# Kernel optimization log

Hardware: AMD Instinct MI355X
Metric: run time of the kernel (lower is better)

Reference implementation:

```python
import jax, jax.numpy as jnp
import numpy as np

RC = 5.0
P = 6
N_ATOM = 4
N_AXIS = 8
EPS = 1e-5
C_RES = 0.89442719  # sqrt(0.8)
C_NEW = 0.4472      # ~sqrt(0.2)
BESSEL_PREF = float(np.sqrt(2.0 / RC))


def poly_cutoff(x):
    # nequip-style PolynomialCutoff, p=6
    xr = x / RC
    p = float(P)
    out = (1.0
           - (p + 1.0) * (p + 2.0) / 2.0 * xr ** P
           + p * (p + 2.0) * xr ** (P + 1)
           - p * (p + 1.0) / 2.0 * xr ** (P + 2))
    return jnp.where(xr < 1.0, out, 0.0)


def bessel(x, w):
    # x: [E], w: [n_basis] (trainable n*pi weights)
    return BESSEL_PREF * jnp.sin(w * x[:, None] / RC) / x[:, None]


def layer_norm(x, g, b):
    m = jnp.mean(x, axis=-1, keepdims=True)
    v = jnp.var(x, axis=-1, keepdims=True)
    return (x - m) * jax.lax.rsqrt(v + EPS) * g + b


def mlp3(x, W1, b1, W2, b2, W3, b3):
    # FFN: hidden block (linear-tanh-linear) + tanh + final linear
    h = jnp.tanh(x @ W1 + b1)
    h = jnp.tanh(h @ W2 + b2)
    return h @ W3 + b3


def resnet3(x, W1, b1, W2, b2, W3, b3):
    # ResNet: residual added where in/out dims match (final 64->64 linear)
    h = jnp.tanh(x @ W1 + b1)
    h = h @ W2 + b2
    return jnp.tanh(h) @ W3 + b3 + h


def seg_mean(x, idx, n):
    s = jax.ops.segment_sum(x, idx, num_segments=n)
    c = jax.ops.segment_sum(jnp.ones((x.shape[0],), x.dtype), idx, num_segments=n)
    c = jnp.maximum(c, 1.0).reshape((n,) + (1,) * (x.ndim - 1))
    return s / c


def setup_inputs() -> dict:
    key = jax.random.key(0)
    ks = iter(jax.random.split(key, 64))
    N, E, E2 = 40000, 320000, 160000
    NB, NR, NS, NA = 16, 64, 16, 8
    D = NA * NS  # 128 = n_hidden
    L = 2
    f32 = jnp.float32

    def nrm(shape, s=0.05):
        return jax.random.normal(next(ks), shape, dtype=f32) * s

    inp = {}
    inp['atom_types'] = jax.random.randint(next(ks), (N,), 0, N_ATOM, dtype=jnp.int32)
    ev = jax.random.normal(next(ks), (E, 3), dtype=f32)
    inp['env_vectors'] = ev
    inp['env_length'] = jnp.linalg.norm(ev, axis=-1) + 0.1
    inp['edge_length'] = jax.random.uniform(next(ks), (E2,), dtype=f32) * 4.0 + 0.5
    inp['env_index'] = jax.random.randint(next(ks), (2, E), 0, N, dtype=jnp.int32)
    inp['edge_index'] = jax.random.randint(next(ks), (2, E2), 0, N, dtype=jnp.int32)
    inp['bessel_w'] = jnp.arange(1, NB + 1, dtype=f32) * jnp.pi
    A = 2 * N_ATOM + NB  # 24
    inp['sr_W1'], inp['sr_b1'] = nrm((A, 64)), nrm((64,))
    inp['sr_W2'], inp['sr_b2'] = nrm((64, 64)), nrm((64,))
    inp['sr_W3'], inp['sr_b3'] = nrm((64, NS)), nrm((NS,))
    inp['rd_W1'], inp['rd_b1'] = nrm((A, 64)), nrm((64,))
    inp['rd_W2'], inp['rd_b2'] = nrm((64, 64)), nrm((64,))
    inp['rd_W3'], inp['rd_b3'] = nrm((64, NR)), nrm((NR,))
    inp['ne_emb_W'], inp['ne_emb_b'] = nrm((NR, D)), nrm((D,))
    inp['ne_nln_g'], inp['ne_nln_b'] = jnp.ones((D,), f32), jnp.zeros((D,), f32)
    inp['ne_eln_g'], inp['ne_eln_b'] = jnp.ones((NR,), f32), jnp.zeros((NR,), f32)
    inp['ly_emb_W'], inp['ly_emb_b'] = nrm((L, NR, D)), nrm((L, D))
    inp['ly_hid_W1'], inp['ly_hid_b1'] = nrm((L, 2 * D, 128)), nrm((L, 128))
    inp['ly_hid_W2'], inp['ly_hid_b2'] = nrm((L, 128, 128)), nrm((L, 128))
    inp['ly_hid_W3'], inp['ly_hid_b3'] = nrm((L, 128, D)), nrm((L, D))
    inp['ly_rdl_W1'], inp['ly_rdl_b1'] = nrm((L, NR + D, 64)), nrm((L, 64))
    inp['ly_rdl_W2'], inp['ly_rdl_b2'] = nrm((L, 64, 64)), nrm((L, 64))
    inp['ly_rdl_W3'], inp['ly_rdl_b3'] = nrm((L, 64, NR)), nrm((L, NR))
    inp['ly_nln_g'], inp['ly_nln_b'] = jnp.ones((L, D), f32), jnp.zeros((L, D), f32)
    inp['ly_eln_g'], inp['ly_eln_b'] = jnp.ones((L, NR), f32), jnp.zeros((L, NR), f32)
    return inp


def reference(atom_types, env_vectors, env_length, edge_length, env_index, edge_index,
              bessel_w,
              sr_W1, sr_b1, sr_W2, sr_b2, sr_W3, sr_b3,
              rd_W1, rd_b1, rd_W2, rd_b2, rd_W3, rd_b3,
              ne_emb_W, ne_emb_b, ne_nln_g, ne_nln_b, ne_eln_g, ne_eln_b,
              ly_emb_W, ly_emb_b,
              ly_hid_W1, ly_hid_b1, ly_hid_W2, ly_hid_b2, ly_hid_W3, ly_hid_b3,
              ly_rdl_W1, ly_rdl_b1, ly_rdl_W2, ly_rdl_b2, ly_rdl_W3, ly_rdl_b3,
              ly_nln_g, ly_nln_b, ly_eln_g, ly_eln_b):
    N = atom_types.shape[0]
    oh = jax.nn.one_hot(atom_types, N_ATOM, dtype=env_vectors.dtype)
    # atom_attr[index].transpose(1,0).reshape(E,-1) == concat of the two endpoints' one-hots
    env_attr = jnp.concatenate([oh[env_index[0]], oh[env_index[1]]], -1)   # [E, 2*n_atom]
    edge_attr = jnp.concatenate([oh[edge_index[0]], oh[edge_index[1]]], -1)
    ud_env = poly_cutoff(env_length)[:, None]    # [E, 1]
    ud_edge = poly_cutoff(edge_length)[:, None]  # [E2, 1]
    feat_env = jnp.concatenate([env_attr, ud_env * bessel(env_length, bessel_w)], -1)
    feat_edge = jnp.concatenate([edge_attr, ud_edge * bessel(edge_length, bessel_w)], -1)
    env_sqrt = mlp3(feat_env, sr_W1, sr_b1, sr_W2, sr_b2, sr_W3, sr_b3) * ud_env  # [E, n_sqrt]
    env_radial = layer_norm(mlp3(feat_env, rd_W1, rd_b1, rd_W2, rd_b2, rd_W3, rd_b3), ne_eln_g, ne_eln_b) * ud_env
    edge_radial = layer_norm(mlp3(feat_edge, rd_W1, rd_b1, rd_W2, rd_b2, rd_W3, rd_b3), ne_eln_g, ne_eln_b) * ud_edge
    # SE(2) aggregation: msg = [env_sqrt | ud * env_vectors]; outer product per node
    msg = env_sqrt[:, :, None] * (ud_env * env_vectors)[:, None, :]  # [E, n_sqrt, 3]
    agg = seg_mean(msg, env_index[1], N)                             # [N, n_sqrt, 3]
    gram = jnp.einsum('nds,nes->nde', agg, agg)[:, :, :N_AXIS]       # [N, n_sqrt, n_axis]
    node_emb = layer_norm(gram.reshape(N, -1), ne_nln_g, ne_nln_b)   # [N, D]
    env_hidden = (env_radial @ ne_emb_W + ne_emb_b) * (node_emb[env_index[1]] + node_emb[env_index[0]]) * 0.5
    edge_hidden = (edge_radial @ ne_emb_W + ne_emb_b) * (node_emb[edge_index[1]] + node_emb[edge_index[0]]) * 0.5
    for l in range(ly_emb_W.shape[0]):
        env_weight = env_radial @ ly_emb_W[l] + ly_emb_b[l]  # [E, D]
        agg2 = seg_mean(env_weight * node_emb[env_index[1]], env_index[1], N)
        node_emb = C_RES * node_emb + C_NEW * layer_norm(agg2, ly_nln_g[l], ly_nln_b[l])
        env_hidden = mlp3(jnp.concatenate([node_emb[env_index[0]], env_hidden], -1),
                          ly_hid_W1[l], ly_hid_b1[l], ly_hid_W2[l], ly_hid_b2[l], ly_hid_W3[l], ly_hid_b3[l])
        edge_hidden = mlp3(jnp.concatenate([node_emb[edge_index[0]], edge_hidden], -1),
                           ly_hid_W1[l], ly_hid_b1[l], ly_hid_W2[l], ly_hid_b2[l], ly_hid_W3[l], ly_hid_b3[l])
        env_radial = C_RES * env_radial + C_NEW * ud_env * layer_norm(
            resnet3(jnp.concatenate([env_radial, env_hidden], -1),
                    ly_rdl_W1[l], ly_rdl_b1[l], ly_rdl_W2[l], ly_rdl_b2[l], ly_rdl_W3[l], ly_rdl_b3[l]),
            ly_eln_g[l], ly_eln_b[l])
        edge_radial = C_RES * edge_radial + C_NEW * ud_edge * layer_norm(
            resnet3(jnp.concatenate([edge_radial, edge_hidden], -1),
                    ly_rdl_W1[l], ly_rdl_b1[l], ly_rdl_W2[l], ly_rdl_b2[l], ly_rdl_W3[l], ly_rdl_b3[l]),
            ly_eln_g[l], ly_eln_b[l])
    return env_radial, edge_radial, node_emb, env_hidden, edge_hidden
```

## Files before the change

kernel.cpp:

```cpp
#include <hip/hip_runtime.h>
#include <math.h>

#define C_RES 0.89442719f
#define C_NEW 0.4472f
#define LN_EPS 1e-5f
#define BESSEL_PREF 0.6324555320336759f
#define RC_INV 0.2f

typedef __attribute__((ext_vector_type(8))) short short8;
typedef __attribute__((ext_vector_type(8))) unsigned short u16x8;
typedef __attribute__((ext_vector_type(16))) float f32x16;

__device__ __forceinline__ float fast_tanh(float x) {
  float t = fminf(3.0f, fmaxf(-3.0f, x));
  float t2 = t * t;
  float num = t * fmaf(t2, 10.0f, 105.0f);
  float den = fmaf(t2, fmaf(t2, 1.0f, 45.0f), 105.0f);
  return num * __builtin_amdgcn_rcpf(den);
}

__device__ __forceinline__ unsigned short f2b(float f) {
  __bf16 h = (__bf16)f;
  return __builtin_bit_cast(unsigned short, h);
}
// ... 330 lines not shown
      float s = v0 + v1, ss = v0*v0 + v1*v1;
      #pragma unroll
      for (int o = 1; o <= 16; o <<= 1) {
        s  += __shfl_xor(s, o);
        ss += __shfl_xor(ss, o);
      }
      const float m   = s * (1.0f/64.0f);
      const float inv = rsqrtf(ss * (1.0f/64.0f) - m*m + LN_EPS);
      const int row32 = (q & 3) + 8*(q >> 2) + 4*(lane >> 5);
      const int rloc  = wave*32 + row32;
      const int row   = base + rloc;
      if (row < nrows) {
        const float u = udl[rloc];
        radial_out[(size_t)row*64 + cl]      = ((v0 - m)*inv*eg0 + eb0) * u;
        radial_out[(size_t)row*64 + 32 + cl] = ((v1 - m)*inv*eg1 + eb1) * u;
      }
    }
  }

  if (has_sr) {
    {
      const float bv0 = srb1[cl], bv1 = srb1[32 + cl];
      #pragma unroll
      for (int q = 0; q < 16; ++q) { acc0[q] = bv0; acc1[q] = bv1; }
    }
    #pragma unroll
    for (int kc = 0; kc < 2; ++kc) {
      const short8 a  = *(const short8*)&afrag[(kc*3 + wave)*512 + swz(lane, kc)*8];
      const short8 w0 = *(const short8*)&wlds[(20 + kc*2 + 0)*512 + lane*8];
      const short8 w1 = *(const short8*)&wlds[(20 + kc*2 + 1)*512 + lane*8];
      acc0 = __builtin_amdgcn_mfma_f32_32x32x16_bf16(a, w0, acc0, 0, 0, 0);
      acc1 = __builtin_amdgcn_mfma_f32_32x32x16_bf16(a, w1, acc1, 0, 0, 0);
    }
    FEAT_TRANS(6, acc0, acc1);

    {
      const float bv0 = srb2[cl], bv1 = srb2[32 + cl];
      #pragma unroll
      for (int q = 0; q < 16; ++q) { acc0[q] = bv0; acc1[q] = bv1; }
    }
    #pragma unroll
    for (int kc = 0; kc < 4; ++kc) {
      const short8 a  = *(const short8*)&afrag[((6 + kc*3) + wave)*512 + swz(lane, kc)*8];
      const short8 w0 = *(const short8*)&wlds[(24 + kc*2 + 0)*512 + lane*8];
      const short8 w1 = *(const short8*)&wlds[(24 + kc*2 + 1)*512 + lane*8];
      acc0 = __builtin_amdgcn_mfma_f32_32x32x16_bf16(a, w0, acc0, 0, 0, 0);
      acc1 = __builtin_amdgcn_mfma_f32_32x32x16_bf16(a, w1, acc1, 0, 0, 0);
    }
    FEAT_TRANS(18, acc0, acc1);

    {
      const float bv0 = (cl < 16) ? srb3[cl] : 0.0f;
      #pragma unroll
      for (int q = 0; q < 16; ++q) acc0[q] = bv0;
    }
    #pragma unroll
    for (int kc = 0; kc < 4; ++kc) {
      const short8 a  = *(const short8*)&afrag[((18 + kc*3) + wave)*512 + swz(lane, kc)*8];
      const short8 w0 = *(const short8*)&wlds[(32 + kc)*512 + lane*8];
      acc0 = __builtin_amdgcn_mfma_f32_32x32x16_bf16(a, w0, acc0, 0, 0, 0);
    }
    if (cl < 16) {
      #pragma unroll
      for (int q = 0; q < 16; ++q) {
        const int row32 = (q & 3) + 8*(q >> 2) + 4*(lane >> 5);
        const int rloc  = wave*32 + row32;
        const int row   = base + rloc;
        if (row < nrows) msgbuf[(size_t)row*20 + cl] = acc0[q] * udl[rloc];
      }
    }
  }
}


__launch_bounds__(256)
__global__ void msg_gather_kernel(int N, const int* __restrict__ eoff,
                                  const int* __restrict__ perm,
                                  const float* __restrict__ msgbuf,
                                  float* __restrict__ aggS)
{
  const int w = (blockIdx.x * 256 + threadIdx.x) >> 6;
  const int lane = threadIdx.x & 63;
  if (w >= N) return;
  const int s = eoff[w], e = eoff[w + 1];
  const int d = lane / 3, c = lane - d * 3;
  float acc = 0.0f;
  for (int j = s; j < e; ++j) {
    const int ed = perm[j];
    if (lane < 48)
      acc += msgbuf[(size_t)ed*20 + d] * msgbuf[(size_t)ed*20 + 16 + c];
  }
  if (lane < 48) aggS[(size_t)w*48 + lane] = acc;
}


__device__ __forceinline__ void block128_stats(float x, float& m, float& inv, float* red) {
  float s = x, ss = x*x;
  #pragma unroll
  for (int o = 32; o; o >>= 1) { s += __shfl_down(s, o); ss += __shfl_down(ss, o); }
  const int t = threadIdx.x;
  if ((t & 63) == 0) { red[(t >> 6)*2] = s; red[(t >> 6)*2 + 1] = ss; }
  __syncthreads();
  const float S = red[0] + red[2], SS = red[1] + red[3];
  m = S * (1.0f/128.0f);
  const float var = SS * (1.0f/128.0f) - m*m;
  inv = rsqrtf(var + LN_EPS);
}

__launch_bounds__(128)
__global__ void node_emb_kernel(int N, const float* __restrict__ aggS,
                                const int* __restrict__ ecnt,
                                const float* __restrict__ g, const float* __restrict__ b,
                                float* __restrict__ node_emb)
{
  const int n = blockIdx.x, t = threadIdx.x;
  __shared__ float S[48];
  __shared__ float red[4];
  if (t < 48) S[t] = aggS[(size_t)n*48 + t];
  __syncthreads();
  const float ic = 1.0f / fmaxf((float)ecnt[n], 1.0f);
  const int d = t >> 3, e = t & 7;
  const float x = (S[d*3+0]*S[e*3+0] + S[d*3+1]*S[e*3+1] + S[d*3+2]*S[e*3+2]) * ic * ic;
  float m, inv;
  block128_stats(x, m, inv, red);
  node_emb[(size_t)n*128 + t] = (x - m)*inv*g[t] + b[t];
}


__launch_bounds__(256)
__global__ void agg_gather_kernel(int N, const int* __restrict__ eoff,
                                  const int* __restrict__ perm,
                                  const float* __restrict__ radial,
                                  float* __restrict__ mean_r)
{
  const int w = (blockIdx.x * 256 + threadIdx.x) >> 6;
  const int lane = threadIdx.x & 63;
  if (w >= N) return;
  const int s = eoff[w], e = eoff[w + 1];
  float acc = 0.0f;
  for (int j = s; j < e; ++j) {
    const int ed = perm[j];
    acc += radial[(size_t)ed * 64 + lane];
  }
  const float inv = 1.0f / fmaxf((float)(e - s), 1.0f);
  mean_r[(size_t)w * 64 + lane] = acc * inv;
}


__launch_bounds__(256)
__global__ void node_update_gemm(
    int N, const float* __restrict__ mean_r, const int* __restrict__ ecnt,
    const float* __restrict__ W, const float* __restrict__ bias,
    const float* __restrict__ g, const float* __restrict__ b,
    float* __restrict__ node_emb)
{
  __shared__ __align__(16) float lw[64*128];
  __shared__ float lm[32][65];
  const int tid = threadIdx.x;
  const int base = blockIdx.x * 32;

  for (int i = tid; i < 8192; i += 256) lw[i] = W[i];
  {
    const int rr0 = tid >> 6, k = tid & 63;
    for (int rr = rr0; rr < 32; rr += 4) {
      const int n = base + rr;
      lm[rr][k] = (n < N) ? mean_r[(size_t)n*64 + k] : 0.0f;
    }
  }
  __syncthreads();

  const int r0 = (tid >> 5) * 4, j0 = (tid & 31) * 4;
  float acc[4][4];
  #pragma unroll
  for (int j = 0; j < 4; ++j) {
    const float bj = bias[j0 + j];
    acc[0][j] = bj; acc[1][j] = bj; acc[2][j] = bj; acc[3][j] = bj;
  }
  for (int k = 0; k < 64; ++k) {
    const float4 w = *(const float4*)&lw[k*128 + j0];
    const float s0 = lm[r0][k],   s1 = lm[r0+1][k];
    const float s2 = lm[r0+2][k], s3 = lm[r0+3][k];
    acc[0][0] += s0*w.x; acc[0][1] += s0*w.y; acc[0][2] += s0*w.z; acc[0][3] += s0*w.w;
    acc[1][0] += s1*w.x; acc[1][1] += s1*w.y; acc[1][2] += s1*w.z; acc[1][3] += s1*w.w;
    acc[2][0] += s2*w.x; acc[2][1] += s2*w.y; acc[2][2] += s2*w.z; acc[2][3] += s2*w.w;
    acc[3][0] += s3*w.x; acc[3][1] += s3*w.y; acc[3][2] += s3*w.z; acc[3][3] += s3*w.w;
  }

  const float g0 = g[j0], g1 = g[j0+1], g2 = g[j0+2], g3 = g[j0+3];
  const float bb0 = b[j0], bb1 = b[j0+1], bb2 = b[j0+2], bb3 = b[j0+3];
  #pragma unroll
  for (int i = 0; i < 4; ++i) {
    const int n = base + r0 + i;
    if (n >= N) continue;
    const float mask = (ecnt[n] > 0) ? 1.0f : 0.0f;
    const float4 old = *(const float4*)&node_emb[(size_t)n*128 + j0];
    const float x0 = old.x * acc[i][0] * mask;
    const float x1 = old.y * acc[i][1] * mask;
    const float x2 = old.z * acc[i][2] * mask;
    const float x3 = old.w * acc[i][3] * mask;
    float s = x0 + x1 + x2 + x3;
    float ss = x0*x0 + x1*x1 + x2*x2 + x3*x3;
    #pragma unroll
    for (int o = 1; o <= 16; o <<= 1) {
      s  += __shfl_xor(s, o);
      ss += __shfl_xor(ss, o);
    }
    const float m = s * (1.0f/128.0f);
    const float inv = rsqrtf(ss * (1.0f/128.0f) - m*m + LN_EPS);
    float4 o4;
    o4.x = C_RES*old.x + C_NEW*((x0 - m)*inv*g0 + bb0);
    o4.y = C_RES*old.y + C_NEW*((x1 - m)*inv*g1 + bb1);
    o4.z = C_RES*old.z + C_NEW*((x2 - m)*inv*g2 + bb2);
    o4.w = C_RES*old.w + C_NEW*((x3 - m)*inv*g3 + bb3);
    *(float4*)&node_emb[(size_t)n*128 + j0] = o4;
  }
}


__launch_bounds__(192)
__global__ void emb_mfma(
    int g1, int n1, const float* __restrict__ radial1, const int* __restrict__ idx1,
    float* __restrict__ out1,
    int n2, const float* __restrict__ radial2, const int* __restrict__ idx2,
    float* __restrict__ out2,
    const unsigned short* __restrict__ wpck, const float* __restrict__ bias,
    const float* __restrict__ node_emb)
{
  __shared__ __align__(16) unsigned short afrag[12*512];
  __shared__ __align__(16) unsigned short wlds[16*512];
  __shared__ int i0l[96], i1l[96];

  const int tid = threadIdx.x, lane = tid & 63, wave = tid >> 6;
  const int cl = lane & 31;

  int blk = blockIdx.x;
  int nrows; const float* radial; const int* idx; float* out;
  if (blk < g1) { nrows = n1; radial = radial1; idx = idx1; out = out1; }
  else { blk -= g1; nrows = n2; radial = radial2; idx = idx2; out = out2; }
  const int base = blk * 96;

  for (int i = tid; i < 1024; i += 192)
    *(u16x8*)&wlds[i*8] = *(const u16x8*)&wpck[i*8];

  {
    const int r = tid >> 1, h = tid & 1;
    int rowg = base + r;
    if (rowg >= nrows) rowg = nrows - 1;
    if (h == 0) { i0l[r] = idx[rowg]; i1l[r] = idx[nrows + rowg]; }
    const float* rsrc = radial + (size_t)rowg * 64;
    #pragma unroll
    for (int g = 0; g < 4; ++g) {
      const int k = h*32 + g*8;
      const u16x8 w = cvt8(rsrc + k);
      const int kc = k >> 4;
      const int s_ = (r & 31) + 32*((k >> 3) & 1);
      *(u16x8*)&afrag[(kc*3 + (r>>5))*512 + swz(s_, kc)*8] = w;
    }
  }
  __syncthreads();

  f32x16 acc0, acc1, acc2, acc3;
  {
    const float bv0 = bias[cl], bv1 = bias[32+cl];
    const float bv2 = bias[64+cl], bv3 = bias[96+cl];
    #pragma unroll
    for (int q = 0; q < 16; ++q) { acc0[q]=bv0; acc1[q]=bv1; acc2[q]=bv2; acc3[q]=bv3; }
  }
  #pragma unroll
  for (int kc = 0; kc < 4; ++kc) {
    const short8 a  = *(const short8*)&afrag[(kc*3 + wave)*512 + swz(lane, kc)*8];
    const short8 w0 = *(const short8*)&wlds[(kc*4 + 0)*512 + lane*8];
    const short8 w1 = *(const short8*)&wlds[(kc*4 + 1)*512 + lane*8];
    const short8 w2 = *(const short8*)&wlds[(kc*4 + 2)*512 + lane*8];
    const short8 w3 = *(const short8*)&wlds[(kc*4 + 3)*512 + lane*8];
    acc0 = __builtin_amdgcn_mfma_f32_32x32x16_bf16(a, w0, acc0, 0, 0, 0);
    acc1 = __builtin_amdgcn_mfma_f32_32x32x16_bf16(a, w1, acc1, 0, 0, 0);
    acc2 = __builtin_amdgcn_mfma_f32_32x32x16_bf16(a, w2, acc2, 0, 0, 0);
    acc3 = __builtin_amdgcn_mfma_f32_32x32x16_bf16(a, w3, acc3, 0, 0, 0);
  }

  #pragma unroll
  for (int q = 0; q < 16; ++q) {
    const int row32 = (q & 3) + 8*(q >> 2) + 4*(lane >> 5);
    const int rloc  = wave*32 + row32;
    const int row   = base + rloc;
    if (row >= nrows) continue;
    const float* n0 = node_emb + (size_t)i0l[rloc]*128;
    const float* n1 = node_emb + (size_t)i1l[rloc]*128;
    float* op = out + (size_t)row*128;
    op[cl]    = acc0[q] * 0.5f * (n0[cl]    + n1[cl]);
    op[32+cl] = acc1[q] * 0.5f * (n0[32+cl] + n1[32+cl]);
    op[64+cl] = acc2[q] * 0.5f * (n0[64+cl] + n1[64+cl]);
    op[96+cl] = acc3[q] * 0.5f * (n0[96+cl] + n1[96+cl]);
  }
}


__launch_bounds__(192)
__global__ void nepre_mfma(int N, const float* __restrict__ node_emb,
                           const unsigned short* __restrict__ wpackh1,
                           const float* __restrict__ hb1,
                           float* __restrict__ nepre)
{
  __shared__ __align__(16) unsigned short afrag[24*512];
  __shared__ __align__(16) unsigned short wlds[32*512];
  const int tid = threadIdx.x, lane = tid & 63, wave = tid >> 6;
  const int cl = lane & 31;
  const int base = blockIdx.x * 96;

  for (int i = tid; i < 2048; i += 192)
    *(u16x8*)&wlds[i*8] = *(const u16x8*)&wpackh1[i*8];

  {
    const int r = tid >> 1, h = tid & 1;
    int rowg = base + r;
    if (rowg >= N) rowg = N - 1;
    const float* s = node_emb + (size_t)rowg * 128;
    #pragma unroll
    for (int g = 0; g < 8; ++g) {
      const int k = h*64 + g*8;
      const u16x8 w = cvt8(s + k);
      const int kc = k >> 4;
      const int s_ = (r & 31) + 32*((k >> 3) & 1);
      *(u16x8*)&afrag[(kc*3 + (r>>5))*512 + swz(s_, kc)*8] = w;
    }
  }
  __syncthreads();

  f32x16 acc0, acc1, acc2, acc3;
  {
    const float bv0 = hb1[cl], bv1 = hb1[32+cl];
    const float bv2 = hb1[64+cl], bv3 = hb1[96+cl];
    #pragma unroll
    for (int q = 0; q < 16; ++q) { acc0[q]=bv0; acc1[q]=bv1; acc2[q]=bv2; acc3[q]=bv3; }
  }
  #pragma unroll
  for (int kc = 0; kc < 8; ++kc) {
    const short8 a  = *(const short8*)&afrag[(kc*3 + wave)*512 + swz(lane, kc)*8];
    const short8 w0 = *(const short8*)&wlds[(kc*4 + 0)*512 + lane*8];
    const short8 w1 = *(const short8*)&wlds[(kc*4 + 1)*512 + lane*8];
    const short8 w2 = *(const short8*)&wlds[(kc*4 + 2)*512 + lane*8];
    const short8 w3 = *(const short8*)&wlds[(kc*4 + 3)*512 + lane*8];
    acc0 = __builtin_amdgcn_mfma_f32_32x32x16_bf16(a, w0, acc0, 0, 0, 0);
    acc1 = __builtin_amdgcn_mfma_f32_32x32x16_bf16(a, w1, acc1, 0, 0, 0);
    acc2 = __builtin_amdgcn_mfma_f32_32x32x16_bf16(a, w2, acc2, 0, 0, 0);
    acc3 = __builtin_amdgcn_mfma_f32_32x32x16_bf16(a, w3, acc3, 0, 0, 0);
  }

  #pragma unroll
  for (int q = 0; q < 16; ++q) {
    const int row32 = (q & 3) + 8*(q >> 2) + 4*(lane >> 5);
    const int row   = base + wave*32 + row32;
    if (row >= N) continue;
    float* op = nepre + (size_t)row*128;
    op[cl]    = acc0[q];
    op[32+cl] = acc1[q];
    op[64+cl] = acc2[q];
    op[96+cl] = acc3[q];
  }
}


#define STAGE_WG(SRC, OFFU16, B) do {                                           \
    _Pragma("unroll")                                                           \
    for (int i_ = 0; i_ < 2; ++i_) {                                            \
      const int c_ = tid + i_*256;                                              \
      *(u16x8*)&wg[B][c_*8] = *(const u16x8*)&(SRC)[(OFFU16) + c_*8];           \
    }                                                                           \
  } while (0)

__launch_bounds__(256, 3)
__global__ void hidrdl_mfma(
    int g1,
    int n1, const int* __restrict__ idx1, const float* __restrict__ ud1,
    float* __restrict__ hid1, float* __restrict__ rad1,
    int n2, const int* __restrict__ idx2, const float* __restrict__ ud2,
    float* __restrict__ hid2, float* __restrict__ rad2,
    const float* __restrict__ nepre,
    const unsigned short* __restrict__ wpackh,
    const float* __restrict__ hb2, const float* __restrict__ hb3,
    const unsigned short* __restrict__ wpackr,
    const float* __restrict__ rb1, const float* __restrict__ rb2,
    const float* __restrict__ rb3,
    const float* __restrict__ eln_g, const float* __restrict__ eln_b)
{
  __shared__ __align__(16) unsigned short afragH[16384];
  __shared__ __align__(16) unsigned short wg[2][4096];

  const int tid  = threadIdx.x;
  const int lane = tid & 63;
  const int wave = tid >> 6;
  const int cl   = lane & 31;
  const int khalf = lane >> 5;

  int blk = blockIdx.x;
  int nrows; const int* idx0; const float* ud; float* hidden; float* radial;
  if (blk < g1) { nrows = n1; idx0 = idx1; ud = ud1; hidden = hid1; radial = rad1; }
  else { blk -= g1; nrows = n2; idx0 = idx2; ud = ud2; hidden = hid2; radial = rad2; }
  const int base = blk * 128;

  int lrow = base + wave*32 + cl;
  if (lrow >= nrows) lrow = nrows - 1;
  const float* hsrc = hidden + (size_t)lrow * 128;
  const float* rsrc = radial + (size_t)lrow * 64;

  short8 aH[8];
  #pragma unroll
  for (int kc = 0; kc < 8; ++kc) aH[kc] = cvt8s(hsrc + kc*16 + khalf*8);

  f32x16 acc[4];

  #pragma unroll
  for (int q = 0; q < 16; ++q) {
    const int row32 = (q & 3) + 8*(q >> 2) + 4*khalf;
    int row = base + wave*32 + row32;
    if (row >= nrows) row = nrows - 1;
    const float* np = nepre + (size_t)idx0[row] * 128;
    acc[0][q] = np[cl];
    acc[1][q] = np[32 + cl];
    acc[2][q] = np[64 + cl];
    acc[3][q] = np[96 + cl];
  }

  STAGE_WG(wpackh, 16384, 0);
  __syncthreads();
  #pragma unroll
  for (int p = 0; p < 4; ++p) {
    if (p < 3) STAGE_WG(wpackh, 16384 + (p+1)*4096, (p+1)&1);
    else       STAGE_WG(wpackh, 32768, 0);
    #pragma unroll
    for (int kcl = 0; kcl < 2; ++kcl) {
      const int kc = p*2 + kcl;
      const short8 a = aH[kc];
      #pragma unroll
      for (int ct = 0; ct < 4; ++ct) {
        const short8 b = *(const short8*)&wg[p&1][ (kcl*4 + ct)*512 + lane*8 ];
        acc[ct] = __builtin_amdgcn_mfma_f32_32x32x16_bf16(a, b, acc[ct], 0, 0, 0);
      }
    }
    __syncthreads();
  }

  #pragma unroll
  for (int ct = 0; ct < 4; ++ct) {
    const int kc  = ct*2 + ((lane >> 4) & 1);
    const int oct = (lane >> 3) & 1;
    const int j   = lane & 7;
    const int xk  = (oct << 1) ^ ((kc & 1) << 2);
    const int hi  = 4*khalf;
    const int bi  = (wave*8 + kc)*512 + oct*256 + j;
    #pragma unroll
    for (int q = 0; q < 16; ++q) {
      const int m32 = (q & 3) + 8*(q >> 2) + hi;
      afragH[bi + (m32 ^ xk)*8] = f2b(fast_tanh(acc[ct][q]));
    }
  }

  #pragma unroll
  for (int ct = 0; ct < 4; ++ct) {
    const float bv = hb2[ct*32 + cl];
    #pragma unroll
    for (int q = 0; q < 16; ++q) acc[ct][q] = bv;
  }
  #pragma unroll
  for (int p = 0; p < 4; ++p) {
    if (p < 3) STAGE_WG(wpackh, 32768 + (p+1)*4096, (p+1)&1);
    else       STAGE_WG(wpackh, 49152, 0);
    #pragma unroll
    for (int kcl = 0; kcl < 2; ++kcl) {
      const int kc = p*2 + kcl;
      const short8 a = *(const short8*)&afragH[ (wave*8 + kc)*512 + swz(lane, kc)*8 ];
      #pragma unroll
      for (int ct = 0; ct < 4; ++ct) {
        const short8 b = *(const short8*)&wg[p&1][ (kcl*4 + ct)*512 + lane*8 ];
        acc[ct] = __builtin_amdgcn_mfma_f32_32x32x16_bf16(a, b, acc[ct], 0, 0, 0);
      }
    }
    __syncthreads();
  }

  #pragma unroll
  for (int ct = 0; ct < 4; ++ct) {
    const int kc  = ct*2 + ((lane >> 4) & 1);
    const int oct = (lane >> 3) & 1;
    const int j   = lane & 7;
    const int xk  = (oct << 1) ^ ((kc & 1) << 2);
    const int hi  = 4*khalf;
    const int bi  = (wave*8 + kc)*512 + oct*256 + j;
    #pragma unroll
    for (int q = 0; q < 16; ++q) {
      const int m32 = (q & 3) + 8*(q >> 2) + hi;
      afragH[bi + (m32 ^ xk)*8] = f2b(fast_tanh(acc[ct][q]));
    }
  }

  #pragma unroll
  for (int ct = 0; ct < 4; ++ct) {
    const float bv = hb3[ct*32 + cl];
    #pragma unroll
    for (int q = 0; q < 16; ++q) acc[ct][q] = bv;
  }
  #pragma unroll
  for (int p = 0; p < 4; ++p) {
    if (p < 3) STAGE_WG(wpackh, 49152 + (p+1)*4096, (p+1)&1);
    else       STAGE_WG(wpackr, 0, 0);
    #pragma unroll
    for (int kcl = 0; kcl < 2; ++kcl) {
      const int kc = p*2 + kcl;
      const short8 a = *(const short8*)&afragH[ (wave*8 + kc)*512 + swz(lane, kc)*8 ];
      #pragma unroll
      for (int ct = 0; ct < 4; ++ct) {
        const short8 b = *(const short8*)&wg[p&1][ (kcl*4 + ct)*512 + lane*8 ];
        acc[ct] = __builtin_amdgcn_mfma_f32_32x32x16_bf16(a, b, acc[ct], 0, 0, 0);
      }
    }
    __syncthreads();
  }

  #pragma unroll
  for (int ct = 0; ct < 4; ++ct) {
    const int col = ct*32 + cl;
    #pragma unroll
    for (int q = 0; q < 16; ++q) {
      const int row = base + wave*32 + (q & 3) + 8*(q >> 2) + 4*khalf;
      if (row < nrows) hidden[(size_t)row*128 + col] = acc[ct][q];
    }
  }
  #pragma unroll
  for (int ct = 0; ct < 4; ++ct) {
    const int kc  = ct*2 + ((lane >> 4) & 1);
    const int oct = (lane >> 3) & 1;
    const int j   = lane & 7;
    const int xk  = (oct << 1) ^ ((kc & 1) << 2);
    const int hi  = 4*khalf;
    const int bi  = (wave*8 + kc)*512 + oct*256 + j;
    #pragma unroll
    for (int q = 0; q < 16; ++q) {
      const int m32 = (q & 3) + 8*(q >> 2) + hi;
      afragH[bi + (m32 ^ xk)*8] = f2b(acc[ct][q]);
    }
  }

  short8 aR[4];
  #pragma unroll
  for (int kc = 0; kc < 4; ++kc) aR[kc] = cvt8s(rsrc + kc*16 + khalf*8);

  f32x16 racc0, racc1;
  {
    const float bv0 = rb1[cl], bv1 = rb1[32 + cl];
    #pragma unroll
    for (int q = 0; q < 16; ++q) { racc0[q] = bv0; racc1[q] = bv1; }
  }
  #pragma unroll
  for (int t = 0; t < 3; ++t) {
    if (t < 2) STAGE_WG(wpackr, (t+1)*4096, (t+1)&1);
    else       STAGE_WG(wpackr, 12288, 1);
    #pragma unroll
    for (int kk = 0; kk < 4; ++kk) {
      const int kc = t*4 + kk;
      const short8 a = (kc < 4) ? aR[kc]
        : *(const short8*)&afragH[ (wave*8 + (kc-4))*512 + swz(lane, kc-4)*8 ];
      const short8 w0 = *(const short8*)&wg[t&1][ (kk*2 + 0)*512 + lane*8 ];
      const short8 w1 = *(const short8*)&wg[t&1][ (kk*2 + 1)*512 + lane*8 ];
      racc0 = __builtin_amdgcn_mfma_f32_32x32x16_bf16(a, w0, racc0, 0, 0, 0);
      racc1 = __builtin_amdgcn_mfma_f32_32x32x16_bf16(a, w1, racc1, 0, 0, 0);
    }
    __syncthreads();
  }

  #pragma unroll
  for (int ct = 0; ct < 2; ++ct) {
    const int colh = ct*32 + cl;
    const int kc2  = colh >> 4;
    const int b3_  = (colh >> 3) & 1;
    const int jj   = colh & 7;
    const int blk2 = (wave*8 + kc2)*512;
    #pragma unroll
    for (int q = 0; q < 16; ++q) {
      const int row32 = (q & 3) + 8*(q >> 2) + 4*khalf;
      const int s_ = (row32 & 31) + 32*b3_;
      const float v = ct ? racc1[q] : racc0[q];
      afragH[blk2 + swz(s_, kc2)*8 + jj] = f2b(fast_tanh(v));
    }
  }

  f32x16 rh0, rh1;
  {
    const float bv0 = rb2[cl], bv1 = rb2[32 + cl];
    #pragma unroll
    for (int q = 0; q < 16; ++q) { rh0[q] = bv0; rh1[q] = bv1; }
  }
  STAGE_WG(wpackr, 16384, 0);
  #pragma unroll
  for (int kc = 0; kc < 4; ++kc) {
    const short8 a  = *(const short8*)&afragH[ (wave*8 + kc)*512 + swz(lane, kc)*8 ];
    const short8 w0 = *(const short8*)&wg[1][ (kc*2 + 0)*512 + lane*8 ];
    const short8 w1 = *(const short8*)&wg[1][ (kc*2 + 1)*512 + lane*8 ];
    rh0 = __builtin_amdgcn_mfma_f32_32x32x16_bf16(a, w0, rh0, 0, 0, 0);
    rh1 = __builtin_amdgcn_mfma_f32_32x32x16_bf16(a, w1, rh1, 0, 0, 0);
  }
  __syncthreads();

  #pragma unroll
  for (int ct = 0; ct < 2; ++ct) {
    const int colh = ct*32 + cl;
    const int kc2  = colh >> 4;
    const int b3_  = (colh >> 3) & 1;
    const int jj   = colh & 7;
    const int blk2 = (wave*8 + 4 + kc2)*512;
    #pragma unroll
    for (int q = 0; q < 16; ++q) {
      const int row32 = (q & 3) + 8*(q >> 2) + 4*khalf;
      const int s_ = (row32 & 31) + 32*b3_;
      const float v = ct ? rh1[q] : rh0[q];
      afragH[blk2 + swz(s_, kc2)*8 + jj] = f2b(fast_tanh(v));
    }
  }

  {
    const float bv0 = rb3[cl], bv1 = rb3[32 + cl];
    #pragma unroll
    for (int q = 0; q < 16; ++q) { racc0[q] = bv0; racc1[q] = bv1; }
  }
  #pragma unroll
  for (int kc = 0; kc < 4; ++kc) {
    const short8 a  = *(const short8*)&afragH[ (wave*8 + 4 + kc)*512 + swz(lane, kc)*8 ];
    const short8 w0 = *(const short8*)&wg[0][ (kc*2 + 0)*512 + lane*8 ];
    const short8 w1 = *(const short8*)&wg[0][ (kc*2 + 1)*512 + lane*8 ];
    racc0 = __builtin_amdgcn_mfma_f32_32x32x16_bf16(a, w0, racc0, 0, 0, 0);
    racc1 = __builtin_amdgcn_mfma_f32_32x32x16_bf16(a, w1, racc1, 0, 0, 0);
  }

  const float eg0 = eln_g[cl],      eb0 = eln_b[cl];
  const float eg1 = eln_g[32 + cl], eb1 = eln_b[32 + cl];
  const float* rtile = radial + (size_t)(base + wave*32) * 64;

  #pragma unroll
  for (int q = 0; q < 16; ++q) {
    const float v0 = racc0[q] + rh0[q];
    const float v1 = racc1[q] + rh1[q];
    float s = v0 + v1, ss = v0*v0 + v1*v1;
    #pragma unroll
    for (int o = 1; o <= 16; o <<= 1) {
      s  += __shfl_xor(s, o);
      ss += __shfl_xor(ss, o);
    }
    const float m   = s * (1.0f/64.0f);
    const float inv = rsqrtf(ss * (1.0f/64.0f) - m*m + LN_EPS);
    const int row32 = (q & 3) + 8*(q >> 2) + 4*khalf;
    const int row   = base + wave*32 + row32;
    if (row < nrows) {
      const float u = ud[row];
      const float oldA = rtile[row32*64 + cl];
      const float oldB = rtile[row32*64 + 32 + cl];
      radial[(size_t)row*64 + cl]      = C_RES*oldA + C_NEW*u*((v0 - m)*inv*eg0 + eb0);
      radial[(size_t)row*64 + 32 + cl] = C_RES*oldB + C_NEW*u*((v1 - m)*inv*eg1 + eb1);
    }
  }
}


extern "C" void kernel_launch(void* const* d_in, const int* in_sizes, int n_in,
                              void* d_out, int out_size, void* d_ws, size_t ws_size,
                              hipStream_t stream)
{
  const int*   atom_types = (const int*)  d_in[0];
  const float* env_vec    = (const float*)d_in[1];
  const float* env_len    = (const float*)d_in[2];
  const float* edge_len   = (const float*)d_in[3];
  const int*   env_idx    = (const int*)  d_in[4];
  const int*   edge_idx   = (const int*)  d_in[5];
  const float* bessel_w   = (const float*)d_in[6];
  const float* srW1 = (const float*)d_in[7];  const float* srb1 = (const float*)d_in[8];
  const float* srW2 = (const float*)d_in[9];  const float* srb2 = (const float*)d_in[10];
  const float* srW3 = (const float*)d_in[11]; const float* srb3 = (const float*)d_in[12];
  const float* rdW1 = (const float*)d_in[13]; const float* rdb1 = (const float*)d_in[14];
  const float* rdW2 = (const float*)d_in[15]; const float* rdb2 = (const float*)d_in[16];
  const float* rdW3 = (const float*)d_in[17]; const float* rdb3 = (const float*)d_in[18];
  const float* ne_emb_W = (const float*)d_in[19]; const float* ne_emb_b = (const float*)d_in[20];
  const float* ne_nln_g = (const float*)d_in[21]; const float* ne_nln_b = (const float*)d_in[22];
  const float* ne_eln_g = (const float*)d_in[23]; const float* ne_eln_b = (const float*)d_in[24];
  const float* ly_emb_W = (const float*)d_in[25]; const float* ly_emb_b = (const float*)d_in[26];
  const float* ly_hid_W1 = (const float*)d_in[27]; const float* ly_hid_b1 = (const float*)d_in[28];
  const float* ly_hid_W2 = (const float*)d_in[29]; const float* ly_hid_b2 = (const float*)d_in[30];
  const float* ly_hid_W3 = (const float*)d_in[31]; const float* ly_hid_b3 = (const float*)d_in[32];
  const float* ly_rdl_W1 = (const float*)d_in[33]; const float* ly_rdl_b1 = (const float*)d_in[34];
  const float* ly_rdl_W2 = (const float*)d_in[35]; const float* ly_rdl_b2 = (const float*)d_in[36];
  const float* ly_rdl_W3 = (const float*)d_in[37]; const float* ly_rdl_b3 = (const float*)d_in[38];
  const float* ly_nln_g = (const float*)d_in[39]; const float* ly_nln_b = (const float*)d_in[40];
  const float* ly_eln_g = (const float*)d_in[41]; const float* ly_eln_b = (const float*)d_in[42];

  const int N  = in_sizes[0];
  const int E  = in_sizes[2];
  const int E2 = in_sizes[3];

  float* out = (float*)d_out;
  float* env_radial  = out;
  float* edge_radial = env_radial + (size_t)E * 64;
  float* node_emb    = edge_radial + (size_t)E2 * 64;
  float* env_hidden  = node_emb + (size_t)N * 128;
  float* edge_hidden = env_hidden + (size_t)E * 128;

  float* ws = (float*)d_ws;
  float* ud_env  = ws;  ws += E;
  float* ud_edge = ws;  ws += E2;
  float* aggS    = ws;  ws += (size_t)N * 48;
  float* msgbuf  = ws;  ws += (size_t)E * 20;
  float* mean_r  = msgbuf;
  float* nepre   = ws;  ws += (size_t)N * 128;
  unsigned short* wpack  = (unsigned short*)ws; ws += 65536;
  unsigned short* wpack2 = (unsigned short*)ws; ws += 20480;
  unsigned short* wpack3 = (unsigned short*)ws; ws += 9216;
  unsigned short* wpackE = (unsigned short*)ws; ws += 4096;
  int* ecnt = (int*)ws; ws += N;
  int* eoff = (int*)ws; ws += N + 1;
  int* ecur = (int*)ws; ws += N + 1;
  int* perm = (int*)ws; ws += E;

  const int gEr  = (E  + 95) / 96;
  const int gE2r = (E2 + 95) / 96;
  const int gEf  = (E  + 127) / 128;
  const int gE2f = (E2 + 127) / 128;
  const int gN32 = (N + 31) / 32;
  const int gN96 = (N + 95) / 96;
  const int gN4w = (N * 64 + 255) / 256;

  zero_int_kernel<<<256, 256, 0, stream>>>(ecnt, N);
  hist_kernel<<<(E + 255) / 256, 256, 0, stream>>>(E, env_idx, ecnt);
  scan_kernel<<<1, 1024, 0, stream>>>(ecnt, eoff, ecur, N);
  scatter_kernel<<<(E + 255) / 256, 256, 0, stream>>>(E, env_idx, ecur, perm);

  pack_hid_weights<<<512, 256, 0, stream>>>(ly_hid_W1, ly_hid_W2, ly_hid_W3, wpack);
  pack_rdl_weights<<<160, 256, 0, stream>>>(ly_rdl_W1, ly_rdl_W2, ly_rdl_W3, wpack2);
  pack_feat_weights<<<72, 256, 0, stream>>>(rdW1, rdW2, rdW3, srW1, srW2, srW3, wpack3);
  pack_emb_weights<<<32, 256, 0, stream>>>(ne_emb_W, wpackE);

  feat_mfma<<<gEr + gE2r, 192, 0, stream>>>(
      gEr, E, env_len, env_idx, env_radial, ud_env,
      E2, edge_len, edge_idx, edge_radial, ud_edge,
      atom_types, env_vec, bessel_w, wpack3,
      srb1, srb2, srb3, rdb1, rdb2, rdb3,
      ne_eln_g, ne_eln_b, msgbuf);

  msg_gather_kernel<<<gN4w, 256, 0, stream>>>(N, eoff, perm, msgbuf, aggS);
  node_emb_kernel<<<N, 128, 0, stream>>>(N, aggS, ecnt, ne_nln_g, ne_nln_b, node_emb);

  emb_mfma<<<gEr + gE2r, 192, 0, stream>>>(
      gEr, E, env_radial, env_idx, env_hidden,
      E2, edge_radial, edge_idx, edge_hidden,
      wpackE, ne_emb_b, node_emb);

  for (int l = 0; l < 2; ++l) {
    agg_gather_kernel<<<gN4w, 256, 0, stream>>>(N, eoff, perm, env_radial, mean_r);
    node_update_gemm<<<gN32, 256, 0, stream>>>(N, mean_r, ecnt,
        ly_emb_W + (size_t)l*64*128, ly_emb_b + (size_t)l*128,
        ly_nln_g + (size_t)l*128, ly_nln_b + (size_t)l*128, node_emb);

    nepre_mfma<<<gN96, 192, 0, stream>>>(N, node_emb,
        wpack + (size_t)l*65536, ly_hid_b1 + (size_t)l*128, nepre);

    hidrdl_mfma<<<gEf + gE2f, 256, 0, stream>>>(
        gEf,
        E, env_idx, ud_env, env_hidden, env_radial,
        E2, edge_idx, ud_edge, edge_hidden, edge_radial,
        nepre,
        wpack + (size_t)l*65536,
        ly_hid_b2 + (size_t)l*128, ly_hid_b3 + (size_t)l*128,
        wpack2 + (size_t)l*20480,
        ly_rdl_b1 + (size_t)l*64, ly_rdl_b2 + (size_t)l*64, ly_rdl_b3 + (size_t)l*64,
        ly_eln_g + (size_t)l*64, ly_eln_b + (size_t)l*64);
  }
}
```

Baseline: 1.095 ms.

## Fuse initial embedding GEMM into first-layer hidden/radial MFMA kernel

```diff
diff --git a/kernel.cpp b/kernel.cpp
--- a/kernel.cpp
+++ b/kernel.cpp
@@ -506,7 +506,7 @@
     int N, const float* __restrict__ mean_r, const int* __restrict__ ecnt,
     const float* __restrict__ W, const float* __restrict__ bias,
     const float* __restrict__ g, const float* __restrict__ b,
-    float* __restrict__ node_emb)
+    const float* __restrict__ nein, float* __restrict__ neout)
 {
   __shared__ __align__(16) float lw[64*128];
   __shared__ float lm[32][65];
@@ -547,7 +547,7 @@
     const int n = base + r0 + i;
     if (n >= N) continue;
     const float mask = (ecnt[n] > 0) ? 1.0f : 0.0f;
-    const float4 old = *(const float4*)&node_emb[(size_t)n*128 + j0];
+    const float4 old = *(const float4*)&nein[(size_t)n*128 + j0];
     const float x0 = old.x * acc[i][0] * mask;
     const float x1 = old.y * acc[i][1] * mask;
     const float x2 = old.z * acc[i][2] * mask;
@@ -566,86 +566,7 @@
     o4.y = C_RES*old.y + C_NEW*((x1 - m)*inv*g1 + bb1);
     o4.z = C_RES*old.z + C_NEW*((x2 - m)*inv*g2 + bb2);
     o4.w = C_RES*old.w + C_NEW*((x3 - m)*inv*g3 + bb3);
-    *(float4*)&node_emb[(size_t)n*128 + j0] = o4;
-  }
-}
-
-
-__launch_bounds__(192)
-__global__ void emb_mfma(
-    int g1, int n1, const float* __restrict__ radial1, const int* __restrict__ idx1,
-    float* __restrict__ out1,
-    int n2, const float* __restrict__ radial2, const int* __restrict__ idx2,
-    float* __restrict__ out2,
-    const unsigned short* __restrict__ wpck, const float* __restrict__ bias,
-    const float* __restrict__ node_emb)
-{
-  __shared__ __align__(16) unsigned short afrag[12*512];
-  __shared__ __align__(16) unsigned short wlds[16*512];
-  __shared__ int i0l[96], i1l[96];
-
-  const int tid = threadIdx.x, lane = tid & 63, wave = tid >> 6;
-  const int cl = lane & 31;
-
-  int blk = blockIdx.x;
-  int nrows; const float* radial; const int* idx; float* out;
-  if (blk < g1) { nrows = n1; radial = radial1; idx = idx1; out = out1; }
-  else { blk -= g1; nrows = n2; radial = radial2; idx = idx2; out = out2; }
-  const int base = blk * 96;
-
-  for (int i = tid; i < 1024; i += 192)
-    *(u16x8*)&wlds[i*8] = *(const u16x8*)&wpck[i*8];
-
-  {
-    const int r = tid >> 1, h = tid & 1;
-    int rowg = base + r;
-    if (rowg >= nrows) rowg = nrows - 1;
-    if (h == 0) { i0l[r] = idx[rowg]; i1l[r] = idx[nrows + rowg]; }
-    const float* rsrc = radial + (size_t)rowg * 64;
-    #pragma unroll
-    for (int g = 0; g < 4; ++g) {
-      const int k = h*32 + g*8;
-      const u16x8 w = cvt8(rsrc + k);
-      const int kc = k >> 4;
-      const int s_ = (r & 31) + 32*((k >> 3) & 1);
-      *(u16x8*)&afrag[(kc*3 + (r>>5))*512 + swz(s_, kc)*8] = w;
-    }
-  }
-  __syncthreads();
-
-  f32x16 acc0, acc1, acc2, acc3;
-  {
-    const float bv0 = bias[cl], bv1 = bias[32+cl];
-    const float bv2 = bias[64+cl], bv3 = bias[96+cl];
-    #pragma unroll
-    for (int q = 0; q < 16; ++q) { acc0[q]=bv0; acc1[q]=bv1; acc2[q]=bv2; acc3[q]=bv3; }
-  }
-  #pragma unroll
-  for (int kc = 0; kc < 4; ++kc) {
-    const short8 a  = *(const short8*)&afrag[(kc*3 + wave)*512 + swz(lane, kc)*8];
-    const short8 w0 = *(const short8*)&wlds[(kc*4 + 0)*512 + lane*8];
-    const short8 w1 = *(const short8*)&wlds[(kc*4 + 1)*512 + lane*8];
-    const short8 w2 = *(const short8*)&wlds[(kc*4 + 2)*512 + lane*8];
-    const short8 w3 = *(const short8*)&wlds[(kc*4 + 3)*512 + lane*8];
-    acc0 = __builtin_amdgcn_mfma_f32_32x32x16_bf16(a, w0, acc0, 0, 0, 0);
-    acc1 = __builtin_amdgcn_mfma_f32_32x32x16_bf16(a, w1, acc1, 0, 0, 0);
-    acc2 = __builtin_amdgcn_mfma_f32_32x32x16_bf16(a, w2, acc2, 0, 0, 0);
-    acc3 = __builtin_amdgcn_mfma_f32_32x32x16_bf16(a, w3, acc3, 0, 0, 0);
-  }
-
-  #pragma unroll
-  for (int q = 0; q < 16; ++q) {
-    const int row32 = (q & 3) + 8*(q >> 2) + 4*(lane >> 5);
-    const int rloc  = wave*32 + row32;
-    const int row   = base + rloc;
-    if (row >= nrows) continue;
-    const float* n0 = node_emb + (size_t)i0l[rloc]*128;
-    const float* n1 = node_emb + (size_t)i1l[rloc]*128;
-    float* op = out + (size_t)row*128;
-    op[cl]    = acc0[q] * 0.5f * (n0[cl]    + n1[cl]);
-    op[32+cl] = acc1[q] * 0.5f * (n0[32+cl] + n1[32+cl]);
-    op[64+cl] = acc2[q] * 0.5f * (n0[64+cl] + n1[64+cl]);
-    op[96+cl] = acc3[q] * 0.5f * (n0[96+cl] + n1[96+cl]);
+    *(float4*)&neout[(size_t)n*128 + j0] = o4;
   }
 }
 
@@ -723,6 +644,25 @@
     }                                                                           \
   } while (0)
 
+#define SCATTER_AFRAGH(ACCARR, DOTANH) do {                                     \
+    _Pragma("unroll")                                                           \
+    for (int ct_ = 0; ct_ < 4; ++ct_) {                                         \
+      const int kc_  = ct_*2 + ((lane >> 4) & 1);                               \
+      const int oct_ = (lane >> 3) & 1;                                         \
+      const int j_   = lane & 7;                                                \
+      const int xk_  = (oct_ << 1) ^ ((kc_ & 1) << 2);                          \
+      const int hi_  = 4*khalf;                                                 \
+      const int bi_  = (wave*8 + kc_)*512 + oct_*256 + j_;                      \
+      _Pragma("unroll")                                                         \
+      for (int q_ = 0; q_ < 16; ++q_) {                                         \
+        const int m32_ = (q_ & 3) + 8*(q_ >> 2) + hi_;                          \
+        const float v_ = (DOTANH) ? fast_tanh(ACCARR[ct_][q_]) : ACCARR[ct_][q_];\
+        afragH[bi_ + (m32_ ^ xk_)*8] = f2b(v_);                                 \
+      }                                                                         \
+    }                                                                           \
+  } while (0)
+
+template<int FIRST>
 __launch_bounds__(256, 3)
 __global__ void hidrdl_mfma(
     int g1,
@@ -731,6 +671,9 @@
     int n2, const int* __restrict__ idx2, const float* __restrict__ ud2,
     float* __restrict__ hid2, float* __restrict__ rad2,
     const float* __restrict__ nepre,
+    const float* __restrict__ ne_old,
+    const unsigned short* __restrict__ wpackE_,
+    const float* __restrict__ embb,
     const unsigned short* __restrict__ wpackh,
     const float* __restrict__ hb2, const float* __restrict__ hb3,
     const unsigned short* __restrict__ wpackr,
@@ -758,11 +701,68 @@
   const float* hsrc = hidden + (size_t)lrow * 128;
   const float* rsrc = radial + (size_t)lrow * 64;
 
+  short8 aR[4];
+  #pragma unroll
+  for (int kc = 0; kc < 4; ++kc) aR[kc] = cvt8s(rsrc + kc*16 + khalf*8);
+
   short8 aH[8];
-  #pragma unroll
-  for (int kc = 0; kc < 8; ++kc) aH[kc] = cvt8s(hsrc + kc*16 + khalf*8);
+  if (!FIRST) {
+    #pragma unroll
+    for (int kc = 0; kc < 8; ++kc) aH[kc] = cvt8s(hsrc + kc*16 + khalf*8);
+  }
 
   f32x16 acc[4];
+
+  if (FIRST) {
+    #pragma unroll
+    for (int ct = 0; ct < 4; ++ct) {
+      const float bv = embb[ct*32 + cl];
+      #pragma unroll
+      for (int q = 0; q < 16; ++q) acc[ct][q] = bv;
+    }
+    STAGE_WG(wpackE_, 0, 0);
+    __syncthreads();
+    STAGE_WG(wpackE_, 4096, 1);
+    #pragma unroll
+    for (int kcl = 0; kcl < 2; ++kcl) {
+      const short8 a = aR[kcl];
+      #pragma unroll
+      for (int ct = 0; ct < 4; ++ct) {
+        const short8 b = *(const short8*)&wg[0][ (kcl*4 + ct)*512 + lane*8 ];
+        acc[ct] = __builtin_amdgcn_mfma_f32_32x32x16_bf16(a, b, acc[ct], 0, 0, 0);
+      }
+    }
+    __syncthreads();
+    STAGE_WG(wpackh, 16384, 0);
+    #pragma unroll
+    for (int kcl = 0; kcl < 2; ++kcl) {
+      const short8 a = aR[2 + kcl];
+      #pragma unroll
+      for (int ct = 0; ct < 4; ++ct) {
+        const short8 b = *(const short8*)&wg[1][ (kcl*4 + ct)*512 + lane*8 ];
+        acc[ct] = __builtin_amdgcn_mfma_f32_32x32x16_bf16(a, b, acc[ct], 0, 0, 0);
+      }
+    }
+    #pragma unroll
+    for (int q = 0; q < 16; ++q) {
+      const int row32 = (q & 3) + 8*(q >> 2) + 4*khalf;
+      int row = base + wave*32 + row32;
+      if (row >= nrows) row = nrows - 1;
+      const int i0 = idx0[row];
+      const int i1 = idx0[nrows + row];
+      const float* n0 = ne_old + (size_t)i0 * 128;
+      const float* n1 = ne_old + (size_t)i1 * 128;
+      acc[0][q] *= 0.5f * (n0[cl]      + n1[cl]);
+      acc[1][q] *= 0.5f * (n0[32 + cl] + n1[32 + cl]);
+      acc[2][q] *= 0.5f * (n0[64 + cl] + n1[64 + cl]);
+      acc[3][q] *= 0.5f * (n0[96 + cl] + n1[96 + cl]);
+    }
+    SCATTER_AFRAGH(acc, false);
+    __syncthreads();
+  } else {
+    STAGE_WG(wpackh, 16384, 0);
+    __syncthreads();
+  }
 
   #pragma unroll
   for (int q = 0; q < 16; ++q) {
@@ -776,8 +776,6 @@
     acc[3][q] = np[96 + cl];
   }
 
-  STAGE_WG(wpackh, 16384, 0);
-  __syncthreads();
   #pragma unroll
   for (int p = 0; p < 4; ++p) {
     if (p < 3) STAGE_WG(wpackh, 16384 + (p+1)*4096, (p+1)&1);
@@ -785,7 +783,9 @@
     #pragma unroll
     for (int kcl = 0; kcl < 2; ++kcl) {
       const int kc = p*2 + kcl;
-      const short8 a = aH[kc];
+      const short8 a = FIRST
+        ? *(const short8*)&afragH[ (wave*8 + kc)*512 + swz(lane, kc)*8 ]
+        : aH[kc];
       #pragma unroll
       for (int ct = 0; ct < 4; ++ct) {
         const short8 b = *(const short8*)&wg[p&1][ (kcl*4 + ct)*512 + lane*8 ];
@@ -795,20 +795,7 @@
     __syncthreads();
   }
 
-  #pragma unroll
-  for (int ct = 0; ct < 4; ++ct) {
-    const int kc  = ct*2 + ((lane >> 4) & 1);
-    const int oct = (lane >> 3) & 1;
-    const int j   = lane & 7;
-    const int xk  = (oct << 1) ^ ((kc & 1) << 2);
-    const int hi  = 4*khalf;
-    const int bi  = (wave*8 + kc)*512 + oct*256 + j;
-    #pragma unroll
-    for (int q = 0; q < 16; ++q) {
-      const int m32 = (q & 3) + 8*(q >> 2) + hi;
-      afragH[bi + (m32 ^ xk)*8] = f2b(fast_tanh(acc[ct][q]));
-    }
-  }
+  SCATTER_AFRAGH(acc, true);
 
   #pragma unroll
   for (int ct = 0; ct < 4; ++ct) {
@@ -833,20 +820,7 @@
     __syncthreads();
   }
 
-  #pragma unroll
-  for (int ct = 0; ct < 4; ++ct) {
-    const int kc  = ct*2 + ((lane >> 4) & 1);
-    const int oct = (lane >> 3) & 1;
-    const int j   = lane & 7;
-    const int xk  = (oct << 1) ^ ((kc & 1) << 2);
-    const int hi  = 4*khalf;
-    const int bi  = (wave*8 + kc)*512 + oct*256 + j;
-    #pragma unroll
-    for (int q = 0; q < 16; ++q) {
-      const int m32 = (q & 3) + 8*(q >> 2) + hi;
-      afragH[bi + (m32 ^ xk)*8] = f2b(fast_tanh(acc[ct][q]));
-    }
-  }
+  SCATTER_AFRAGH(acc, true);
 
   #pragma unroll
   for (int ct = 0; ct < 4; ++ct) {
@@ -880,24 +854,7 @@
       if (row < nrows) hidden[(size_t)row*128 + col] = acc[ct][q];
     }
   }
-  #pragma unroll
-  for (int ct = 0; ct < 4; ++ct) {
-    const int kc  = ct*2 + ((lane >> 4) & 1);
-    const int oct = (lane >> 3) & 1;
-    const int j   = lane & 7;
-    const int xk  = (oct << 1) ^ ((kc & 1) << 2);
-    const int hi  = 4*khalf;
-    const int bi  = (wave*8 + kc)*512 + oct*256 + j;
-    #pragma unroll
-    for (int q = 0; q < 16; ++q) {
-      const int m32 = (q & 3) + 8*(q >> 2) + hi;
-      afragH[bi + (m32 ^ xk)*8] = f2b(acc[ct][q]);
-    }
-  }
-
-  short8 aR[4];
-  #pragma unroll
-  for (int kc = 0; kc < 4; ++kc) aR[kc] = cvt8s(rsrc + kc*16 + khalf*8);
+  SCATTER_AFRAGH(acc, false);
 
   f32x16 racc0, racc1;
   {
@@ -1060,7 +1017,8 @@
   float* ud_edge = ws;  ws += E2;
   float* aggS    = ws;  ws += (size_t)N * 48;
   float* msgbuf  = ws;  ws += (size_t)E * 20;
-  float* mean_r  = msgbuf;
+  float* mean_r  = aggS;
+  float* nemb2   = aggS + (size_t)N * 64;
   float* nepre   = ws;  ws += (size_t)N * 128;
   unsigned short* wpack  = (unsigned short*)ws; ws += 65536;
   unsigned short* wpack2 = (unsigned short*)ws; ws += 20480;
@@ -1099,29 +1057,33 @@
   msg_gather_kernel<<<gN4w, 256, 0, stream>>>(N, eoff, perm, msgbuf, aggS);
   node_emb_kernel<<<N, 128, 0, stream>>>(N, aggS, ecnt, ne_nln_g, ne_nln_b, node_emb);
 
-  emb_mfma<<<gEr + gE2r, 192, 0, stream>>>(
-      gEr, E, env_radial, env_idx, env_hidden,
-      E2, edge_radial, edge_idx, edge_hidden,
-      wpackE, ne_emb_b, node_emb);
-
-  for (int l = 0; l < 2; ++l) {
-    agg_gather_kernel<<<gN4w, 256, 0, stream>>>(N, eoff, perm, env_radial, mean_r);
-    node_update_gemm<<<gN32, 256, 0, stream>>>(N, mean_r, ecnt,
-        ly_emb_W + (size_t)l*64*128, ly_emb_b + (size_t)l*128,
-        ly_nln_g + (size_t)l*128, ly_nln_b + (size_t)l*128, node_emb);
-
-    nepre_mfma<<<gN96, 192, 0, stream>>>(N, node_emb,
-        wpack + (size_t)l*65536, ly_hid_b1 + (size_t)l*128, nepre);
-
-    hidrdl_mfma<<<gEf + gE2f, 256, 0, stream>>>(
-        gEf,
-        E, env_idx, ud_env, env_hidden, env_radial,
-        E2, edge_idx, ud_edge, edge_hidden, edge_radial,
-        nepre,
-        wpack + (size_t)l*65536,
-        ly_hid_b2 + (size_t)l*128, ly_hid_b3 + (size_t)l*128,
-        wpack2 + (size_t)l*20480,
-        ly_rdl_b1 + (size_t)l*64, ly_rdl_b2 + (size_t)l*64, ly_rdl_b3 + (size_t)l*64,
-        ly_eln_g + (size_t)l*64, ly_eln_b + (size_t)l*64);
-  }
-}
+  agg_gather_kernel<<<gN4w, 256, 0, stream>>>(N, eoff, perm, env_radial, mean_r);
+  node_update_gemm<<<gN32, 256, 0, stream>>>(N, mean_r, ecnt,
+      ly_emb_W, ly_emb_b, ly_nln_g, ly_nln_b, node_emb, nemb2);
+  nepre_mfma<<<gN96, 192, 0, stream>>>(N, nemb2, wpack, ly_hid_b1, nepre);
+  hidrdl_mfma<1><<<gEf + gE2f, 256, 0, stream>>>(
+      gEf,
+      E, env_idx, ud_env, env_hidden, env_radial,
+      E2, edge_idx, ud_edge, edge_hidden, edge_radial,
+      nepre,
+      node_emb, wpackE, ne_emb_b,
+      wpack, ly_hid_b2, ly_hid_b3,
+      wpack2, ly_rdl_b1, ly_rdl_b2, ly_rdl_b3,
+      ly_eln_g, ly_eln_b);
+
+  agg_gather_kernel<<<gN4w, 256, 0, stream>>>(N, eoff, perm, env_radial, mean_r);
+  node_update_gemm<<<gN32, 256, 0, stream>>>(N, mean_r, ecnt,
+      ly_emb_W + (size_t)64*128, ly_emb_b + 128,
+      ly_nln_g + 128, ly_nln_b + 128, nemb2, node_emb);
+  nepre_mfma<<<gN96, 192, 0, stream>>>(N, node_emb, wpack + 65536,
+      ly_hid_b1 + 128, nepre);
+  hidrdl_mfma<0><<<gEf + gE2f, 256, 0, stream>>>(
+      gEf,
+      E, env_idx, ud_env, env_hidden, env_radial,
+      E2, edge_idx, ud_edge, edge_hidden, edge_radial,
+      nepre,
+      nullptr, nullptr, nullptr,
+      wpack + 65536, ly_hid_b2 + 128, ly_hid_b3 + 128,
+      wpack2 + 20480, ly_rdl_b1 + 64, ly_rdl_b2 + 64, ly_rdl_b3 + 64,
+      ly_eln_g + 64, ly_eln_b + 64);
+}
```

After: 1.119 ms. 1.02x slower.
